# Kernel optimization log

Measured on AMD Instinct MI355X. Metric: run time of the kernel, lower is better.

Reference implementation:

```python
import jax, jax.numpy as jnp
import numpy as np

DIM = 1024
NUM_HEADS = 16
HEAD_DIM = DIM // NUM_HEADS
SCALE = DIM ** (-0.5)  # NOTE: original scales by full dim, not head_dim


def setup_inputs() -> dict:
    key = jax.random.key(0)
    ks = jax.random.split(key, 5)
    B, S = 2, 2048
    x = jax.random.normal(ks[0], (B, S, DIM), dtype=jnp.float32)
    w_qkv = jax.random.normal(ks[1], (DIM, 3 * DIM), dtype=jnp.float32) * (DIM ** -0.5)
    b_qkv = jax.random.normal(ks[2], (3 * DIM,), dtype=jnp.float32) * 0.02
    w_proj = jax.random.normal(ks[3], (DIM, DIM), dtype=jnp.float32) * (DIM ** -0.5)
    b_proj = jax.random.normal(ks[4], (DIM,), dtype=jnp.float32) * 0.02
    return {"x": x, "w_qkv": w_qkv, "b_qkv": b_qkv, "w_proj": w_proj, "b_proj": b_proj}


def reference(x, w_qkv, b_qkv, w_proj, b_proj):
    B, S, D = x.shape
    qkv = x @ w_qkv + b_qkv                                  # [B,S,3D]
    qkv = qkv.reshape(B, S, NUM_HEADS, 3 * HEAD_DIM).transpose(0, 2, 1, 3)  # [B,H,S,3hd]
    q, k, v = jnp.split(qkv, 3, axis=-1)                     # each [B,H,S,hd]
    attn = jnp.einsum("bhqd,bhkd->bhqk", q, k) * SCALE       # [B,H,S,S]
    attn = jax.nn.softmax(attn, axis=-1)
    out = jnp.einsum("bhqk,bhkd->bhqd", attn, v)             # [B,H,S,hd]
    out = out.transpose(0, 2, 1, 3).reshape(B, S, D)
    return out @ w_proj + b_proj
```

## Files before the change

kernel.cpp:

```cpp
#include <hip/hip_runtime.h>
#include <hip/hip_bf16.h>

#define DIM 1024
#define NH 16
#define HD 64
#define BB 2
#define SS 2048
#define MROWS (BB * SS)
#define SCALE 0.03125f
#define SC_LOG2E 0.04508422002778011f

typedef unsigned short u16;
typedef unsigned int u32;
typedef __attribute__((ext_vector_type(8))) short short8;
typedef __attribute__((ext_vector_type(4))) float f32x4;
typedef __attribute__((ext_vector_type(2))) unsigned int u32x2;

#if __has_builtin(__builtin_amdgcn_exp2f)
#define EXP2(x) __builtin_amdgcn_exp2f(x)
#else
#define EXP2(x) __builtin_exp2f(x)
#endif

__device__ __forceinline__ u16 f2bf(float f) {
  union { float f; u32 u; } v; v.f = f;
  return (u16)((v.u + 0x7fffu + ((v.u >> 16) & 1u)) >> 16);
}

__device__ __forceinline__ u32 pack2bf(float a, float b) {
  union { __hip_bfloat162 h; u32 u; } cv;
  cv.h = __float22bfloat162_rn(make_float2(a, b));
  return cv.u;
}

__device__ __forceinline__ void plswap32(u32& a, u32& b) {
#if __has_builtin(__builtin_amdgcn_permlane32_swap)
  u32x2 t = __builtin_amdgcn_permlane32_swap(a, b, false, false);
  a = t[0]; b = t[1];
#else
  asm("v_permlane32_swap_b32 %0, %1" : "+v"(a), "+v"(b));
#endif
}
__device__ __forceinline__ void plswap16(u32& a, u32& b) {
#if __has_builtin(__builtin_amdgcn_permlane16_swap)
  u32x2 t = __builtin_amdgcn_permlane16_swap(a, b, false, false);
  a = t[0]; b = t[1];
#else
  asm("v_permlane16_swap_b32 %0, %1" : "+v"(a), "+v"(b));
#endif
}

__device__ __forceinline__ void async16(const u16* g, u16* l) {
  __builtin_amdgcn_global_load_lds(
      (const __attribute__((address_space(1))) void*)(const void*)g,
      (__attribute__((address_space(3))) void*)(void*)l, 16, 0, 0);
}

__device__ __forceinline__ short8 ld8(const u16* p) { return *(const short8*)p; }

__global__ void cvt_kernel(const float* __restrict__ in, u16* __restrict__ out, int n4) {
  int i = blockIdx.x * blockDim.x + threadIdx.x;
  if (i < n4) {
    float4 v = ((const float4*)in)[i];
    u32 lo = (u32)f2bf(v.x) | ((u32)f2bf(v.y) << 16);
    u32 hi = (u32)f2bf(v.z) | ((u32)f2bf(v.w) << 16);
    ((uint2*)out)[i] = make_uint2(lo, hi);
  }
}

__global__ void tconv_kernel(const float* __restrict__ in, u16* __restrict__ out, int R, int C) {
  __shared__ u16 t[64 * 65];
  int c0 = blockIdx.x * 64, r0 = blockIdx.y * 64;
  #pragma unroll
  for (int i = 0; i < 16; i++) {
    int j = i * 256 + threadIdx.x;
    int rr = j >> 6, cc = j & 63;
    t[rr * 65 + cc] = f2bf(in[(size_t)(r0 + rr) * C + c0 + cc]);
  }
  __syncthreads();
  #pragma unroll
  for (int i = 0; i < 16; i++) {
    int j = i * 256 + threadIdx.x;
    int oc = j >> 6, orr = j & 63;
    out[(size_t)(c0 + oc) * R + r0 + orr] = t[orr * 65 + oc];
  }
}

template <int MODE>
__global__ __launch_bounds__(256, 2) void gemm_bt(
    const u16* __restrict__ A, const u16* __restrict__ Bt,
    const float* __restrict__ bias, void* __restrict__ C,
    u16* __restrict__ vT, int M, int N, int K) {
  __shared__ __align__(16) u16 As[128 * 32];
  __shared__ __align__(16) u16 Bs[128 * 32];
  const int tid = threadIdx.x;
  const int w = tid >> 6, l = tid & 63;
  const int r = l & 15, q = l >> 4;
  const int m0 = blockIdx.y * 128, n0 = blockIdx.x * 128;
  const int qm = (w & 1) * 64, qn = (w >> 1) * 64;

  const size_t aoff = (size_t)(m0 + w * 16 + (l >> 2)) * K + (size_t)(l & 3) * 8;
  const size_t boff = (size_t)(n0 + w * 16 + (l >> 2)) * K + (size_t)(l & 3) * 8;
  u16* alds = &As[(w * 64 + l) * 8];
  u16* blds = &Bs[(w * 64 + l) * 8];

  f32x4 acc[4][4] = {};
  for (int k0 = 0; k0 < K; k0 += 32) {
    async16(A + aoff + k0, alds);
    async16(A + aoff + (size_t)64 * K + k0, alds + 2048);
    async16(Bt + boff + k0, blds);
    async16(Bt + boff + (size_t)64 * K + k0, blds + 2048);
    __syncthreads();
    short8 af[4], bfr[4];
    #pragma unroll
    for (int i = 0; i < 4; i++) af[i] = ld8(&As[(qm + i * 16 + r) * 32 + q * 8]);
    #pragma unroll
    for (int j = 0; j < 4; j++) bfr[j] = ld8(&Bs[(qn + j * 16 + r) * 32 + q * 8]);
    #pragma unroll
    for (int i = 0; i < 4; i++)
      #pragma unroll
      for (int j = 0; j < 4; j++)
        acc[i][j] = __builtin_amdgcn_mfma_f32_16x16x32_bf16(af[i], bfr[j], acc[i][j], 0, 0, 0);
    __syncthreads();
  }
  #pragma unroll
  for (int i = 0; i < 4; i++) {
    int ro = m0 + qm + i * 16 + q * 4;
    #pragma unroll
    for (int j = 0; j < 4; j++) {
      int col = n0 + qn + j * 16 + r;
      float bv = bias[col];
      float v0 = acc[i][j][0] + bv, v1 = acc[i][j][1] + bv;
      float v2 = acc[i][j][2] + bv, v3 = acc[i][j][3] + bv;
      if (MODE == 1) {
        float* out = (float*)C;
        out[(size_t)(ro + 0) * N + col] = v0;
        out[(size_t)(ro + 1) * N + col] = v1;
        out[(size_t)(ro + 2) * N + col] = v2;
        out[(size_t)(ro + 3) * N + col] = v3;
      } else {
        int h = col / 192, wi = col - h * 192;
        if (wi >= 128) {
          int bb = ro >> 11, s = ro & 2047, d = wi - 128;
          uint2 pk = make_uint2(pack2bf(v0, v1), pack2bf(v2, v3));
          *(uint2*)&vT[((size_t)((bb * NH + h) * HD + d)) * SS + s] = pk;
        } else {
          u16* qk2 = (u16*)C;
          const float sc = (wi < 64) ? SC_LOG2E : 1.0f;
          qk2[(size_t)(ro + 0) * 2048 + h * 128 + wi] = f2bf(v0 * sc);
          qk2[(size_t)(ro + 1) * 2048 + h * 128 + wi] = f2bf(v1 * sc);
          qk2[(size_t)(ro + 2) * 2048 + h * 128 + wi] = f2bf(v2 * sc);
          qk2[(size_t)(ro + 3) * 2048 + h * 128 + wi] = f2bf(v3 * sc);
        }
      }
    }
  }
}

__global__ __launch_bounds__(512, 4) void attn5_kernel(
    const u16* __restrict__ qk2, const u16* __restrict__ vT,
    u16* __restrict__ attno) {
  __shared__ __align__(16) u16 smem[32768];
  const int tid = threadIdx.x;
  const int w = tid >> 6, l = tid & 63;
  const int r = l & 15, q = l >> 4;
  const int wq = w & 3, ws = w >> 2;
  const int b = blockIdx.z, h = blockIdx.y, q0 = blockIdx.x * 128;

  const u16* qb = qk2 + (size_t)b * SS * 2048;
  const u16* kB = qb + h * 128 + 64;
  const u16* vB = vT + (size_t)((b * NH + h) * HD) * SS;

  short8 qf[2][2];
  #pragma unroll
  for (int i = 0; i < 2; i++)
    #pragma unroll
    for (int kq = 0; kq < 2; kq++)
      qf[i][kq] = ld8(qb + (size_t)(q0 + wq * 32 + i * 16 + r) * 2048 + h * 128 + kq * 32 + q * 8);

  const int klrow = l >> 3;
  const int kchunk = (l & 7) ^ klrow;
  const int vlrow = l >> 4;
  const int vslot = l & 15;

#define STAGE(KV0, DST) do {                                                     \
    u16* Kd_ = (DST); u16* Vd_ = Kd_ + 8192;                                     \
    _Pragma("unroll")                                                            \
    for (int tt = 0; tt < 2; tt++) {                                             \
      int g = w * 2 + tt;                                                        \
      async16(kB + (size_t)((KV0) + g * 8 + klrow) * 2048 + kchunk * 8,          \
              &Kd_[g * 512 + l * 8]);                                            \
    }                                                                            \
    _Pragma("unroll")                                                            \
    for (int tt = 0; tt < 2; tt++) {                                             \
      int g = w * 2 + tt;                                                        \
      int d_ = g * 4 + vlrow;                                                    \
      int c_ = vslot ^ (d_ & 15);                                                \
      async16(vB + (size_t)d_ * SS + (KV0) + c_ * 8, &Vd_[g * 512 + l * 8]);     \
    }                                                                            \
  } while (0)

  const short8 vone = {0x3F80, 0x3F80, 0x3F80, 0x3F80, 0x3F80, 0x3F80, 0x3F80, 0x3F80};
  f32x4 oacc[2][4] = {};
  f32x4 den[2] = {};

  STAGE(0, smem);
  __syncthreads();

  for (int t = 0; t < 16; ++t) {
    const int cur = t & 1;
    u16* Ks = smem + cur * 16384;
    u16* Vs = Ks + 8192;
    if (t < 15) STAGE((t + 1) * 128, smem + (cur ^ 1) * 16384);

    f32x4 sacc[4][2] = {};
    #pragma unroll
    for (int j2 = 0; j2 < 4; j2++) {
      const u16* krow = &Ks[(ws * 64 + j2 * 16 + r) * 64];
      short8 a0 = ld8(krow + ((q ^ (r & 7)) * 8));
      short8 a1 = ld8(krow + (((4 + q) ^ (r & 7)) * 8));
      #pragma unroll
      for (int i = 0; i < 2; i++) {
        sacc[j2][i] = __builtin_amdgcn_mfma_f32_16x16x32_bf16(a0, qf[i][0], sacc[j2][i], 0, 0, 0);
        sacc[j2][i] = __builtin_amdgcn_mfma_f32_16x16x32_bf16(a1, qf[i][1], sacc[j2][i], 0, 0, 0);
      }
    }
    short8 pa[2][2];
    #pragma unroll
    for (int ks = 0; ks < 2; ks++)
      #pragma unroll
      for (int i = 0; i < 2; i++) {
        f32x4 sa = sacc[ks * 2][i], sb = sacc[ks * 2 + 1][i];
        u32 A0 = pack2bf(EXP2(sa[0]), EXP2(sa[1]));
        u32 A1 = pack2bf(EXP2(sa[2]), EXP2(sa[3]));
        u32 B0 = pack2bf(EXP2(sb[0]), EXP2(sb[1]));
        u32 B1 = pack2bf(EXP2(sb[2]), EXP2(sb[3]));
        plswap32(A0, B0);
        plswap32(A1, B1);
        plswap16(A0, B0);
        plswap16(A1, B1);
        union { short8 s8; u32 u[4]; } pk;
        pk.u[0] = A0; pk.u[1] = A1; pk.u[2] = B0; pk.u[3] = B1;
        pa[ks][i] = pk.s8;
      }
    #pragma unroll
    for (int ks = 0; ks < 2; ks++) {
      den[0] = __builtin_amdgcn_mfma_f32_16x16x32_bf16(pa[ks][0], vone, den[0], 0, 0, 0);
      den[1] = __builtin_amdgcn_mfma_f32_16x16x32_bf16(pa[ks][1], vone, den[1], 0, 0, 0);
      #pragma unroll
      for (int dj = 0; dj < 4; dj++) {
        short8 vb = ld8(&Vs[(dj * 16 + r) * 128 + (((ws * 8 + ks * 4 + q) ^ r) * 8)]);
        oacc[0][dj] = __builtin_amdgcn_mfma_f32_16x16x32_bf16(pa[ks][0], vb, oacc[0][dj], 0, 0, 0);
        oacc[1][dj] = __builtin_amdgcn_mfma_f32_16x16x32_bf16(pa[ks][1], vb, oacc[1][dj], 0, 0, 0);
      }
    }
    __syncthreads();
  }
#undef STAGE

  float* part = (float*)smem;
  float* dnf  = part + 8 * 32 * 36;
  const int ho = 1 - ws;
  {
    const int wbase = (wq * 2 + ho) * 32;
    #pragma unroll
    for (int i = 0; i < 2; i++) {
      if (ws == 0) {
        *(f32x4*)&part[(wbase + r) * 36 + i * 16 + q * 4]      = oacc[i][2];
        *(f32x4*)&part[(wbase + 16 + r) * 36 + i * 16 + q * 4] = oacc[i][3];
      } else {
        *(f32x4*)&part[(wbase + r) * 36 + i * 16 + q * 4]      = oacc[i][0];
        *(f32x4*)&part[(wbase + 16 + r) * 36 + i * 16 + q * 4] = oacc[i][1];
      }
      if (r == 0)
        *(f32x4*)&dnf[(ws * 4 + wq) * 32 + i * 16 + q * 4] = den[i];
    }
  }
  __syncthreads();
  {
    const int rbase = (wq * 2 + ws) * 32;
    #pragma unroll
    for (int i = 0; i < 2; i++) {
      f32x4 dt = *(f32x4*)&dnf[(ho * 4 + wq) * 32 + i * 16 + q * 4] + den[i];
      f32x4 oa, ob;
      if (ws == 0) { oa = oacc[i][0]; ob = oacc[i][1]; }
      else         { oa = oacc[i][2]; ob = oacc[i][3]; }
      oa += *(f32x4*)&part[(rbase + r) * 36 + i * 16 + q * 4];
      ob += *(f32x4*)&part[(rbase + 16 + r) * 36 + i * 16 + q * 4];
      #pragma unroll
      for (int e = 0; e < 4; e++) {
        float di = 1.f / dt[e];
        int row = q0 + wq * 32 + i * 16 + q * 4 + e;
        u16* o = &attno[(size_t)(b * SS + row) * DIM + h * HD + ws * 32 + r];
        o[0]  = f2bf(oa[e] * di);
        o[16] = f2bf(ob[e] * di);
      }
    }
  }
}

extern "C" void kernel_launch(void* const* d_in, const int* in_sizes, int n_in,
                              void* d_out, int out_size, void* d_ws, size_t ws_size,
                              hipStream_t stream) {
  const float* x      = (const float*)d_in[0];
  const float* w_qkv  = (const float*)d_in[1];
  const float* b_qkv  = (const float*)d_in[2];
  const float* w_proj = (const float*)d_in[3];
  const float* b_proj = (const float*)d_in[4];
  float* out = (float*)d_out;
  char* ws = (char*)d_ws;
  u16* xb     = (u16*)(ws);
  u16* wqkvT  = (u16*)(ws + ((size_t)8  << 20));
  u16* wprojT = (u16*)(ws + ((size_t)14 << 20));
  u16* qk2    = (u16*)(ws + ((size_t)16 << 20));
  u16* attno  = (u16*)(ws + ((size_t)32 << 20));
  u16* vT     = (u16*)(ws + ((size_t)40 << 20));

  cvt_kernel<<<4096, 256, 0, stream>>>(x, xb, MROWS * DIM / 4);
  tconv_kernel<<<dim3(48, 16), 256, 0, stream>>>(w_qkv, wqkvT, DIM, 3 * DIM);
  tconv_kernel<<<dim3(16, 16), 256, 0, stream>>>(w_proj, wprojT, DIM, DIM);
  gemm_bt<0><<<dim3(24, 32), 256, 0, stream>>>(xb, wqkvT, b_qkv, qk2, vT, MROWS, 3 * DIM, DIM);
  attn5_kernel<<<dim3(16, NH, BB), 512, 0, stream>>>(qk2, vT, attno);
  gemm_bt<1><<<dim3(8, 32), 256, 0, stream>>>(attno, wprojT, b_proj, out, nullptr, MROWS, DIM, DIM);
}
```

Before: 191.3 us.

## Interleave QK/exp/PV stages in attention and remap block indices for locality

Reorders the attention inner loop so the exp/pack conversion of the first key half overlaps with the MFMA work of the second half and with PV, instead of running the three phases strictly one after another. It wraps MFMA groups in s_setprio so waves issuing matrix ops get priority. It also remaps block IDs so that consecutive workgroups cover different (batch, head) pairs in groups of 8, which is meant to change how K/V reuse lands in L2 across XCDs. The cost is extra live registers for the overlapped work and a scheduling result that depends on the compiler.

```diff
diff --git a/kernel.cpp b/kernel.cpp
--- a/kernel.cpp
+++ b/kernel.cpp
@@ -157,7 +157,7 @@
   }
 }
 
-__global__ __launch_bounds__(512, 4) void attn5_kernel(
+__global__ __launch_bounds__(512, 4) void attn6_kernel(
     const u16* __restrict__ qk2, const u16* __restrict__ vT,
     u16* __restrict__ attno) {
   __shared__ __align__(16) u16 smem[32768];
@@ -165,7 +165,11 @@
   const int w = tid >> 6, l = tid & 63;
   const int r = l & 15, q = l >> 4;
   const int wq = w & 3, ws = w >> 2;
-  const int b = blockIdx.z, h = blockIdx.y, q0 = blockIdx.x * 128;
+  const int lin = blockIdx.x + 16 * (blockIdx.y + 16 * blockIdx.z);
+  const int k8 = lin & 7, jj = lin >> 3;
+  const int bh = ((jj >> 4) << 3) + k8;
+  const int h = bh & 15, b = bh >> 4;
+  const int q0 = (jj & 15) * 128;
 
   const u16* qb = qk2 + (size_t)b * SS * 2048;
   const u16* kB = qb + h * 128 + 64;
@@ -200,6 +204,50 @@
     }                                                                            \
   } while (0)
 
+#define CONV(ks) do {                                                            \
+    _Pragma("unroll")                                                            \
+    for (int i = 0; i < 2; i++) {                                                \
+      f32x4 sa = sacc[(ks) * 2][i], sb = sacc[(ks) * 2 + 1][i];                  \
+      u32 A0 = pack2bf(EXP2(sa[0]), EXP2(sa[1]));                                \
+      u32 A1 = pack2bf(EXP2(sa[2]), EXP2(sa[3]));                                \
+      u32 B0 = pack2bf(EXP2(sb[0]), EXP2(sb[1]));                                \
+      u32 B1 = pack2bf(EXP2(sb[2]), EXP2(sb[3]));                                \
+      plswap32(A0, B0);                                                          \
+      plswap32(A1, B1);                                                          \
+      plswap16(A0, B0);                                                          \
+      plswap16(A1, B1);                                                          \
+      union { short8 s8; u32 u[4]; } pk;                                         \
+      pk.u[0] = A0; pk.u[1] = A1; pk.u[2] = B0; pk.u[3] = B1;                    \
+      pa[ks][i] = pk.s8;                                                         \
+    }                                                                            \
+  } while (0)
+
+#define QKT(j2) do {                                                             \
+    const u16* krow = &Ks[(ws * 64 + (j2) * 16 + r) * 64];                       \
+    short8 a0 = ld8(krow + ((q ^ (r & 7)) * 8));                                 \
+    short8 a1 = ld8(krow + (((4 + q) ^ (r & 7)) * 8));                           \
+    __builtin_amdgcn_s_setprio(1);                                               \
+    _Pragma("unroll")                                                            \
+    for (int i = 0; i < 2; i++) {                                                \
+      sacc[j2][i] = __builtin_amdgcn_mfma_f32_16x16x32_bf16(a0, qf[i][0], sacc[j2][i], 0, 0, 0); \
+      sacc[j2][i] = __builtin_amdgcn_mfma_f32_16x16x32_bf16(a1, qf[i][1], sacc[j2][i], 0, 0, 0); \
+    }                                                                            \
+    __builtin_amdgcn_s_setprio(0);                                               \
+  } while (0)
+
+#define PV(ks) do {                                                              \
+    __builtin_amdgcn_s_setprio(1);                                               \
+    den[0] = __builtin_amdgcn_mfma_f32_16x16x32_bf16(pa[ks][0], vone, den[0], 0, 0, 0); \
+    den[1] = __builtin_amdgcn_mfma_f32_16x16x32_bf16(pa[ks][1], vone, den[1], 0, 0, 0); \
+    _Pragma("unroll")                                                            \
+    for (int dj = 0; dj < 4; dj++) {                                             \
+      short8 vb = ld8(&Vs[(dj * 16 + r) * 128 + (((ws * 8 + (ks) * 4 + q) ^ r) * 8)]); \
+      oacc[0][dj] = __builtin_amdgcn_mfma_f32_16x16x32_bf16(pa[ks][0], vb, oacc[0][dj], 0, 0, 0); \
+      oacc[1][dj] = __builtin_amdgcn_mfma_f32_16x16x32_bf16(pa[ks][1], vb, oacc[1][dj], 0, 0, 0); \
+    }                                                                            \
+    __builtin_amdgcn_s_setprio(0);                                               \
+  } while (0)
+
   const short8 vone = {0x3F80, 0x3F80, 0x3F80, 0x3F80, 0x3F80, 0x3F80, 0x3F80, 0x3F80};
   f32x4 oacc[2][4] = {};
   f32x4 den[2] = {};
@@ -214,49 +262,19 @@
     if (t < 15) STAGE((t + 1) * 128, smem + (cur ^ 1) * 16384);
 
     f32x4 sacc[4][2] = {};
-    #pragma unroll
-    for (int j2 = 0; j2 < 4; j2++) {
-      const u16* krow = &Ks[(ws * 64 + j2 * 16 + r) * 64];
-      short8 a0 = ld8(krow + ((q ^ (r & 7)) * 8));
-      short8 a1 = ld8(krow + (((4 + q) ^ (r & 7)) * 8));
-      #pragma unroll
-      for (int i = 0; i < 2; i++) {
-        sacc[j2][i] = __builtin_amdgcn_mfma_f32_16x16x32_bf16(a0, qf[i][0], sacc[j2][i], 0, 0, 0);
-        sacc[j2][i] = __builtin_amdgcn_mfma_f32_16x16x32_bf16(a1, qf[i][1], sacc[j2][i], 0, 0, 0);
-      }
-    }
     short8 pa[2][2];
-    #pragma unroll
-    for (int ks = 0; ks < 2; ks++)
-      #pragma unroll
-      for (int i = 0; i < 2; i++) {
-        f32x4 sa = sacc[ks * 2][i], sb = sacc[ks * 2 + 1][i];
-        u32 A0 = pack2bf(EXP2(sa[0]), EXP2(sa[1]));
-        u32 A1 = pack2bf(EXP2(sa[2]), EXP2(sa[3]));
-        u32 B0 = pack2bf(EXP2(sb[0]), EXP2(sb[1]));
-        u32 B1 = pack2bf(EXP2(sb[2]), EXP2(sb[3]));
-        plswap32(A0, B0);
-        plswap32(A1, B1);
-        plswap16(A0, B0);
-        plswap16(A1, B1);
-        union { short8 s8; u32 u[4]; } pk;
-        pk.u[0] = A0; pk.u[1] = A1; pk.u[2] = B0; pk.u[3] = B1;
-        pa[ks][i] = pk.s8;
-      }
-    #pragma unroll
-    for (int ks = 0; ks < 2; ks++) {
-      den[0] = __builtin_amdgcn_mfma_f32_16x16x32_bf16(pa[ks][0], vone, den[0], 0, 0, 0);
-      den[1] = __builtin_amdgcn_mfma_f32_16x16x32_bf16(pa[ks][1], vone, den[1], 0, 0, 0);
-      #pragma unroll
-      for (int dj = 0; dj < 4; dj++) {
-        short8 vb = ld8(&Vs[(dj * 16 + r) * 128 + (((ws * 8 + ks * 4 + q) ^ r) * 8)]);
-        oacc[0][dj] = __builtin_amdgcn_mfma_f32_16x16x32_bf16(pa[ks][0], vb, oacc[0][dj], 0, 0, 0);
-        oacc[1][dj] = __builtin_amdgcn_mfma_f32_16x16x32_bf16(pa[ks][1], vb, oacc[1][dj], 0, 0, 0);
-      }
-    }
+    QKT(0); QKT(1);
+    CONV(0);
+    QKT(2); QKT(3);
+    PV(0);
+    CONV(1);
+    PV(1);
     __syncthreads();
   }
 #undef STAGE
+#undef CONV
+#undef QKT
+#undef PV
 
   float* part = (float*)smem;
   float* dnf  = part + 8 * 32 * 36;
@@ -320,6 +338,6 @@
   tconv_kernel<<<dim3(48, 16), 256, 0, stream>>>(w_qkv, wqkvT, DIM, 3 * DIM);
   tconv_kernel<<<dim3(16, 16), 256, 0, stream>>>(w_proj, wprojT, DIM, DIM);
   gemm_bt<0><<<dim3(24, 32), 256, 0, stream>>>(xb, wqkvT, b_qkv, qk2, vT, MROWS, 3 * DIM, DIM);
-  attn5_kernel<<<dim3(16, NH, BB), 512, 0, stream>>>(qk2, vT, attno);
+  attn6_kernel<<<dim3(16, NH, BB), 512, 0, stream>>>(qk2, vT, attno);
   gemm_bt<1><<<dim3(8, 32), 256, 0, stream>>>(attno, wprojT, b_proj, out, nullptr, MROWS, DIM, DIM);
 }
```

New measurement: 189.1 us. No clear change (-1.2%).
